# Kernel tuning notes

Measured on AMD Instinct MI355X. Metric: run time of the kernel, lower is better.

## Reference

```python
import jax, jax.numpy as jnp
import numpy as np

N_NODES = 33
EPS = 1e-5


def _tconv(x, w, b):
    # x: (B,T,N,Ci); w: (3,O,Ci,1,ks); b: (3,O). Gated temporal conv: relu(P*sigmoid(Q)+R)
    xt = jnp.transpose(x, (0, 3, 2, 1))  # (B,Ci,N,T)
    def c(i):
        y = jax.lax.conv_general_dilated(xt, w[i], (1, 1), 'VALID',
                                         dimension_numbers=('NCHW', 'OIHW', 'NCHW'))
        return y + b[i][None, :, None, None]
    P, Q, R = c(0), c(1), c(2)
    H = jax.nn.relu(P * jax.nn.sigmoid(Q) + R)
    return jnp.transpose(H, (0, 3, 2, 1))  # (B,T',N,O)


def _cheb(x, edge_index, Wk, bias):
    # ChebConv K=3, sym normalization, lambda_max=2 => L_hat = -D^{-1/2} A D^{-1/2} (diag cancels)
    src, tgt = edge_index[0], edge_index[1]
    w = jnp.ones((src.shape[0],), x.dtype)
    deg = jnp.zeros((N_NODES,), x.dtype).at[src].add(w)
    dinv = jnp.where(deg > 0, deg ** -0.5, 0.0)
    lap_w = -dinv[src] * w * dinv[tgt]

    def prop(z):  # z: (B,T,N,C); sparse matvec over edges, aggregate at target
        zg = z[:, :, src, :] * lap_w[None, None, :, None]
        return jnp.zeros_like(z).at[:, :, tgt, :].add(zg)

    Tx0 = x
    Tx1 = prop(Tx0)
    Tx2 = 2.0 * prop(Tx1) - Tx0
    out = (jnp.einsum('btnc,cd->btnd', Tx0, Wk[0])
           + jnp.einsum('btnc,cd->btnd', Tx1, Wk[1])
           + jnp.einsum('btnc,cd->btnd', Tx2, Wk[2]))
    return out + bias


def _bn(x, g, b):
    # BatchNorm2d(num_nodes): stats per node over (B,T,C); biased variance, train-mode stats
    mean = x.mean(axis=(0, 1, 3), keepdims=True)
    var = x.var(axis=(0, 1, 3), keepdims=True)
    return (x - mean) * jax.lax.rsqrt(var + EPS) * g[None, None, :, None] + b[None, None, :, None]


def _stconv(x, ei, tc1w, tc1b, cw, cb, tc2w, tc2b, bng, bnb):
    t = _tconv(x, tc1w, tc1b)
    t = jax.nn.relu(_cheb(t, ei, cw, cb))
    t = _tconv(t, tc2w, tc2b)
    return _bn(t, bng, bnb)


def setup_inputs() -> dict:
    key = jax.random.key(0)
    ks = jax.random.split(key, 24)
    s = 0.05
    inp = {
        'x': jax.random.normal(ks[0], (32, 512, 33, 3), jnp.float32),
        'edge_index': jax.random.randint(ks[1], (2, 64), 0, 33, jnp.int64) if jax.config.jax_enable_x64 else jax.random.randint(ks[1], (2, 64), 0, 33).astype(jnp.int32),
        # STConv 1 (in=3, hid=out=64)
        's1_tc1_w': jax.random.normal(ks[2], (3, 64, 3, 1, 3), jnp.float32) * s,
        's1_tc1_b': jax.random.normal(ks[3], (3, 64), jnp.float32) * s,
        's1_cheb_w': jax.random.normal(ks[4], (3, 64, 64), jnp.float32) * s,
        's1_cheb_b': jax.random.normal(ks[5], (64,), jnp.float32) * s,
        's1_tc2_w': jax.random.normal(ks[6], (3, 64, 64, 1, 3), jnp.float32) * s,
        's1_tc2_b': jax.random.normal(ks[7], (3, 64), jnp.float32) * s,
        's1_bn_g': jnp.ones((33,), jnp.float32),
        's1_bn_b': jnp.zeros((33,), jnp.float32),
        # STConv 2 (in=64, hid=out=64)
        's2_tc1_w': jax.random.normal(ks[8], (3, 64, 64, 1, 3), jnp.float32) * s,
        's2_tc1_b': jax.random.normal(ks[9], (3, 64), jnp.float32) * s,
        's2_cheb_w': jax.random.normal(ks[10], (3, 64, 64), jnp.float32) * s,
        's2_cheb_b': jax.random.normal(ks[11], (64,), jnp.float32) * s,
        's2_tc2_w': jax.random.normal(ks[12], (3, 64, 64, 1, 3), jnp.float32) * s,
        's2_tc2_b': jax.random.normal(ks[13], (3, 64), jnp.float32) * s,
        's2_bn_g': jnp.ones((33,), jnp.float32),
        's2_bn_b': jnp.zeros((33,), jnp.float32),
        # classifier: Linear(64*33 -> 256), Linear(256 -> 10)
        'fc1_w': jax.random.normal(ks[14], (64 * 33, 256), jnp.float32) * s,
        'fc1_b': jax.random.normal(ks[15], (256,), jnp.float32) * s,
        'fc2_w': jax.random.normal(ks[16], (256, 10), jnp.float32) * s,
        'fc2_b': jax.random.normal(ks[17], (10,), jnp.float32) * s,
    }
    return inp


def reference(x, edge_index,
              s1_tc1_w, s1_tc1_b, s1_cheb_w, s1_cheb_b, s1_tc2_w, s1_tc2_b, s1_bn_g, s1_bn_b,
              s2_tc1_w, s2_tc1_b, s2_cheb_w, s2_cheb_b, s2_tc2_w, s2_tc2_b, s2_bn_g, s2_bn_b,
              fc1_w, fc1_b, fc2_w, fc2_b):
    h = jax.nn.relu(_stconv(x, edge_index, s1_tc1_w, s1_tc1_b, s1_cheb_w, s1_cheb_b,
                            s1_tc2_w, s1_tc2_b, s1_bn_g, s1_bn_b))
    h = jax.nn.relu(_stconv(h, edge_index, s2_tc1_w, s2_tc1_b, s2_cheb_w, s2_cheb_b,
                            s2_tc2_w, s2_tc2_b, s2_bn_g, s2_bn_b))
    h = h.mean(axis=1)                      # (B, N, C) mean over time
    h = h.reshape(h.shape[0], -1)           # (B, N*C)
    h = jax.nn.relu(h @ fc1_w + fc1_b)      # dropout = identity (eval)
    return h @ fc2_w + fc2_b                # (B, num_classes)
```

## Files before the change

kernel.cpp:

```cpp
#include <hip/hip_runtime.h>
#include <math.h>

#define NN 33
#define NC 2112

typedef __attribute__((ext_vector_type(8))) short bfrag;
typedef __attribute__((ext_vector_type(4))) float f32x4;

#define OFF_LT   0
#define OFF_L2T  2244
#define OFF_UP1  4488
#define OFF_UP2  16776
#define OFF_WT0  29064
#define OFF_WT1  65928
#define OFF_WT2  102792
#define OFF_ST1  139656
#define OFF_ST2  139722
#define OFF_HB   139856
#define OFF_MEAN 148048
#define OFF_A    215632
#define A_ELEMS  34332672ull
#define SLAB     1077120ull

__device__ inline unsigned short f2bf(float x) {
  unsigned int u = __float_as_uint(x);
  unsigned int r = (u + 0x7fffu + ((u >> 16) & 1u)) >> 16;
  return (unsigned short)r;
}
__device__ inline float bf2f(unsigned short h) {
  return __uint_as_float(((unsigned int)h) << 16);
}

__global__ __launch_bounds__(256) void k_prep_lap(
    const int* __restrict__ ei, float* __restrict__ ws) {
  __shared__ float Lsm[1089];
  __shared__ float L2sm[1089];
  __shared__ float deg[NN];
  __shared__ float dinv[NN];
  int tid = threadIdx.x;
  for (int i = tid; i < 1089; i += 256) Lsm[i] = 0.f;
  if (tid < NN) deg[tid] = 0.f;
  __syncthreads();
  if (tid < 64) atomicAdd(&deg[ei[tid]], 1.f);
  __syncthreads();
  if (tid < NN) dinv[tid] = deg[tid] > 0.f ? rsqrtf(deg[tid]) : 0.f;
  __syncthreads();
  if (tid < 64) {
    int s = ei[tid], t = ei[64 + tid];
    atomicAdd(&Lsm[t * NN + s], -dinv[s] * dinv[t]);
  }
  __syncthreads();
  for (int i = tid; i < 1089; i += 256) {
    int r = i / NN, c = i % NN;
    float s = 0.f;
    for (int m = 0; m < NN; m++) s += Lsm[r * NN + m] * Lsm[m * NN + c];
    L2sm[i] = 2.f * s;
  }
  __syncthreads();
  for (int i = tid; i < 33 * 66; i += 256) {
    int m = i / 66, nn = i % 66;
    int n33 = nn < 33 ? nn : nn - 33;
    ws[OFF_LT + m * 68 + nn]  = Lsm[n33 * NN + m];
    ws[OFF_L2T + m * 68 + nn] = L2sm[n33 * NN + m];
  }
}

__global__ __launch_bounds__(256) void k_prep_w(
    const float* __restrict__ cw1, const float* __restrict__ cw2,
    const float* __restrict__ tw0, const float* __restrict__ tw1,
    const float* __restrict__ tw2, float* __restrict__ ws) {
  int u = blockIdx.x * 256 + threadIdx.x;
  if (u < 24576) {
    unsigned short* u1 = (unsigned short*)(ws + OFF_UP1);
    unsigned short* u2 = (unsigned short*)(ws + OFF_UP2);
    int j = u & 7;
    int nn = (u >> 3) & 15;
    int q = (u >> 7) & 3;
    int sp = (u >> 9) & 1;
    int blk = u >> 10;
    int nt = blk & 3;
    int ks = blk >> 2;
    int k = ks * 32 + q * 8 + j;
    int d = nt * 16 + nn;
    int s = k >> 6, cc = k & 63;
    float v1 = cw1[(s * 64 + cc) * 64 + d];
    float v2 = cw2[(s * 64 + cc) * 64 + d];
    if (s == 0) { v1 -= cw1[(128 + cc) * 64 + d]; v2 -= cw2[(128 + cc) * 64 + d]; }
    unsigned short h1 = f2bf(v1);
    u1[u] = sp ? f2bf(v1 - bf2f(h1)) : h1;
    unsigned short h2 = f2bf(v2);
    u2[u] = sp ? f2bf(v2 - bf2f(h2)) : h2;
  }
  {
    unsigned short* p0 = (unsigned short*)(ws + OFF_WT0);
    unsigned short* p1 = (unsigned short*)(ws + OFF_WT1);
    unsigned short* p2 = (unsigned short*)(ws + OFF_WT2);
    int j  = u & 7;
    int nn_ = (u >> 3) & 15;
    int q  = (u >> 7) & 3;
    int B  = u >> 9;
    int sp = B & 1;
    int B2 = B >> 1;
    int nt = B2 % 12;
    int dk = B2 / 12;
    int ks = dk & 1;
    int dt = dk >> 1;
    int o  = nt * 16 + nn_;
    int ci = ks * 32 + q * 8 + j;
    int src = (o * 64 + ci) * 3 + dt;
    float w0 = tw0[src], w1 = tw1[src], w2 = tw2[src];
    unsigned short h;
    h = f2bf(w0); p0[u] = sp ? f2bf(w0 - bf2f(h)) : h;
    h = f2bf(w1); p1[u] = sp ? f2bf(w1 - bf2f(h)) : h;
    h = f2bf(w2); p2[u] = sp ? f2bf(w2 - bf2f(h)) : h;
  }
}

__global__ __launch_bounds__(256) void k_tconv0(
    const float* __restrict__ x, const float* __restrict__ w,
    const float* __restrict__ bias, float* __restrict__ out,
    int b0, int total) {
  __shared__ float wsm[1728];
  __shared__ float bsm[192];
  int tid = threadIdx.x;
  for (int i = tid; i < 1728; i += 256) wsm[i] = w[i];
  if (tid < 192) bsm[tid] = bias[tid];
  __syncthreads();
  int idx = blockIdx.x * 256 + tid;
  if (idx >= total) return;
  int ch = idx & 63;
  int r = idx >> 6;
  int n = r % NN; r /= NN;
  int t = r % 510;
  int bc = r / 510;
  int b = b0 + bc;
  float aP = bsm[ch], aQ = bsm[64 + ch], aR = bsm[128 + ch];
  const float* xp = x + ((size_t)(b * 512 + t) * NN + n) * 3;
  #pragma unroll
  for (int dt = 0; dt < 3; dt++) {
    float x0 = xp[dt * 99 + 0], x1 = xp[dt * 99 + 1], x2 = xp[dt * 99 + 2];
    aP += x0 * wsm[(ch * 3 + 0) * 3 + dt] + x1 * wsm[(ch * 3 + 1) * 3 + dt] + x2 * wsm[(ch * 3 + 2) * 3 + dt];
    aQ += x0 * wsm[((64 + ch) * 3 + 0) * 3 + dt] + x1 * wsm[((64 + ch) * 3 + 1) * 3 + dt] + x2 * wsm[((64 + ch) * 3 + 2) * 3 + dt];
    aR += x0 * wsm[((128 + ch) * 3 + 0) * 3 + dt] + x1 * wsm[((128 + ch) * 3 + 1) * 3 + dt] + x2 * wsm[((128 + ch) * 3 + 2) * 3 + dt];
  }
  float sg = 1.f / (1.f + __expf(-aQ));
  out[(size_t)(bc * 510 + t) * NC + n * 64 + ch] = fmaxf(aP * sg + aR, 0.f);
}

__global__ __launch_bounds__(256, 4) void k_chebmm(
    const float* __restrict__ in, const unsigned short* __restrict__ Uf,
    const float* __restrict__ cbias, float* __restrict__ out,
    const float* __restrict__ ws, int totalRows) {
  __shared__ __attribute__((aligned(16))) unsigned short Zh[64 * 136];
  __shared__ __attribute__((aligned(16))) unsigned short Zl[64 * 136];

  int tid = threadIdx.x;
  int R0 = blockIdx.x * 64;
  int c = tid & 63;
  int g = __builtin_amdgcn_readfirstlane(tid >> 6);
  int Rg = R0 + g * 16;
  int btg = Rg / 33;
  int n0 = Rg - btg * 33;
  int wrap = 33 - n0;

  const float* lt  = ws + OFF_LT;
  const float* l2t = ws + OFF_L2T;
  const float* ipA = in + (size_t)btg * NC + c;
  const float* ipB = ipA + NC;
  float z1[16], z2[16];
  #pragma unroll
  for (int rr = 0; rr < 16; rr++) { z1[rr] = 0.f; z2[rr] = 0.f; }
  #pragma unroll 11
  for (int m = 0; m < NN; m++) {
    float hvA = ipA[m * 64];
    float hvB = ipB[m * 64];
    const float* ltm  = lt + m * 68 + n0;
    const float* l2tm = l2t + m * 68 + n0;
    #pragma unroll
    for (int rr = 0; rr < 16; rr++) {
      float hv = (rr < wrap) ? hvA : hvB;
      z1[rr] += ltm[rr] * hv;
      z2[rr] += l2tm[rr] * hv;
    }
  }
  #pragma unroll
  for (int rr = 0; rr < 16; rr++) {
    int r = g * 16 + rr;
    unsigned short zh1 = f2bf(z1[rr]);
    Zh[r * 136 + c] = zh1;
    Zl[r * 136 + c] = f2bf(z1[rr] - bf2f(zh1));
    unsigned short zh2 = f2bf(z2[rr]);
    Zh[r * 136 + 64 + c] = zh2;
    Zl[r * 136 + 64 + c] = f2bf(z2[rr] - bf2f(zh2));
  }

  int lane = tid & 63;
  int m15 = lane & 15, q = lane >> 4;
  f32x4 acc[4];
  #pragma unroll
  for (int nt = 0; nt < 4; nt++) acc[nt] = (f32x4){0.f, 0.f, 0.f, 0.f};

  const float* hrow = in + (size_t)(Rg + m15) * 64 + q * 8;
  float hv0[8], hv1[8];
  *(float4*)&hv0[0] = *(const float4*)(hrow);
  *(float4*)&hv0[4] = *(const float4*)(hrow + 4);
  *(float4*)&hv1[0] = *(const float4*)(hrow + 32);
  *(float4*)&hv1[4] = *(const float4*)(hrow + 36);

  bfrag uh[4], ul[4];
  #pragma unroll
  for (int nt = 0; nt < 4; nt++) {
    const unsigned short* bp = Uf + nt * 1024 + lane * 8;
    uh[nt] = *(const bfrag*)bp;
    ul[nt] = *(const bfrag*)(bp + 512);
  }

  #pragma unroll
  for (int ks = 0; ks < 6; ks++) {
    bfrag nh[4], nl[4];
    if (ks < 5) {
      #pragma unroll
      for (int nt = 0; nt < 4; nt++) {
        const unsigned short* bp = Uf + ((ks + 1) * 4 + nt) * 1024 + lane * 8;
        nh[nt] = *(const bfrag*)bp;
        nl[nt] = *(const bfrag*)(bp + 512);
      }
    }
    bfrag ah, al;
    if (ks < 2) {
      const float* hv = (ks == 0) ? hv0 : hv1;
      union { bfrag v; unsigned short s[8]; } Ahf, Alf;
      #pragma unroll
      for (int j = 0; j < 8; j++) {
        unsigned short hh = f2bf(hv[j]);
        Ahf.s[j] = hh;
        Alf.s[j] = f2bf(hv[j] - bf2f(hh));
      }
      ah = Ahf.v; al = Alf.v;
    } else {
      int aoff = (g * 16 + m15) * 136 + (ks - 2) * 32 + q * 8;
      ah = *(const bfrag*)(Zh + aoff);
      al = *(const bfrag*)(Zl + aoff);
    }
    #pragma unroll
    for (int nt = 0; nt < 4; nt++) {
      acc[nt] = __builtin_amdgcn_mfma_f32_16x16x32_bf16(ah, uh[nt], acc[nt], 0, 0, 0);
      acc[nt] = __builtin_amdgcn_mfma_f32_16x16x32_bf16(ah, ul[nt], acc[nt], 0, 0, 0);
      acc[nt] = __builtin_amdgcn_mfma_f32_16x16x32_bf16(al, uh[nt], acc[nt], 0, 0, 0);
    }
    #pragma unroll
    for (int nt = 0; nt < 4; nt++) { uh[nt] = nh[nt]; ul[nt] = nl[nt]; }
  }
  #pragma unroll
  for (int nt = 0; nt < 4; nt++) {
    int d = nt * 16 + m15;
    float bd = cbias[d];
    #pragma unroll
    for (int rr = 0; rr < 4; rr++) {
      int R = R0 + g * 16 + q * 4 + rr;
      if (R < totalRows)
        out[(size_t)R * 64 + d] = fmaxf(acc[nt][rr] + bd, 0.f);
    }
  }
}

__global__ __launch_bounds__(256, 4) void k_tconv(
    const float* __restrict__ in, int inStride, int Tin,
    const unsigned short* __restrict__ wsp, const float* __restrict__ bias,
    float* __restrict__ out, int outStride, int Tout,
    const float* __restrict__ bnSt, const float* __restrict__ bnG,
    const float* __restrict__ bnB, float bnCnt, float* __restrict__ statsOut) {
  __shared__ __attribute__((aligned(16))) unsigned short Ah[34 * 72];
  __shared__ __attribute__((aligned(16))) unsigned short Al[34 * 72];
  __shared__ float red[8];
  int tid = threadIdx.x;
  int ntt = (Tout + 31) >> 5;
  int tpb = NN * ntt;
  int bc = blockIdx.x / tpb, r = blockIdx.x % tpb;
  int n = r / ntt, tt = r % ntt;
  int t0 = tt << 5;
  const float* ip = in + (size_t)bc * inStride * NC + n * 64;

  float sc = 1.f, sh = 0.f;
  if (bnSt) {
    float mean = bnSt[n] / bnCnt;
    float var = bnSt[33 + n] / bnCnt - mean * mean;
    sc = rsqrtf(var + 1e-5f) * bnG[n];
    sh = bnB[n] - mean * sc;
  }
  for (int i = tid; i < 34 * 16; i += 256) {
    int row = i >> 4, c4 = i & 15;
    float4 v = make_float4(0.f, 0.f, 0.f, 0.f);
    if (t0 + row < Tin) v = *(const float4*)(ip + (size_t)(t0 + row) * NC + c4 * 4);
    if (bnSt) {
      v.x = fmaxf(v.x * sc + sh, 0.f);
      v.y = fmaxf(v.y * sc + sh, 0.f);
      v.z = fmaxf(v.z * sc + sh, 0.f);
      v.w = fmaxf(v.w * sc + sh, 0.f);
    }
    unsigned short h0 = f2bf(v.x), h1 = f2bf(v.y), h2 = f2bf(v.z), h3 = f2bf(v.w);
    unsigned short l0 = f2bf(v.x - bf2f(h0)), l1 = f2bf(v.y - bf2f(h1));
    unsigned short l2 = f2bf(v.z - bf2f(h2)), l3 = f2bf(v.w - bf2f(h3));
    uint2 ph, pl;
    ph.x = (unsigned)h0 | ((unsigned)h1 << 16); ph.y = (unsigned)h2 | ((unsigned)h3 << 16);
    pl.x = (unsigned)l0 | ((unsigned)l1 << 16); pl.y = (unsigned)l2 | ((unsigned)l3 << 16);
    *(uint2*)(Ah + row * 72 + c4 * 4) = ph;
    *(uint2*)(Al + row * 72 + c4 * 4) = pl;
  }
  __syncthreads();

  int lane = tid & 63;
  int wv = tid >> 6;
  int m15 = lane & 15, q = lane >> 4;

  f32x4 acc[2][3];
  #pragma unroll
  for (int mi = 0; mi < 2; mi++)
    #pragma unroll
    for (int j = 0; j < 3; j++) acc[mi][j] = (f32x4){0.f, 0.f, 0.f, 0.f};

  #pragma unroll
  for (int s = 0; s < 6; s++) {
    int dt = s >> 1, ks = s & 1;
    const unsigned short* wdt = wsp + (size_t)dt * 24576;
    bfrag bh[3], bl[3];
    #pragma unroll
    for (int j = 0; j < 3; j++) {
      int nt = wv + 4 * j;
      const unsigned short* bp = wdt + ((ks * 12 + nt) * 2) * 512 + lane * 8;
      bh[j] = *(const bfrag*)bp;
      bl[j] = *(const bfrag*)(bp + 512);
    }
    bfrag ah[2], al[2];
    #pragma unroll
    for (int mi = 0; mi < 2; mi++) {
      int row = mi * 16 + m15 + dt;
      int off = row * 72 + ks * 32 + q * 8;
      ah[mi] = *(const bfrag*)(Ah + off);
      al[mi] = *(const bfrag*)(Al + off);
    }
    #pragma unroll
    for (int j = 0; j < 3; j++)
      #pragma unroll
      for (int mi = 0; mi < 2; mi++) {
        acc[mi][j] = __builtin_amdgcn_mfma_f32_16x16x32_bf16(ah[mi], bh[j], acc[mi][j], 0, 0, 0);
        acc[mi][j] = __builtin_amdgcn_mfma_f32_16x16x32_bf16(ah[mi], bl[j], acc[mi][j], 0, 0, 0);
        acc[mi][j] = __builtin_amdgcn_mfma_f32_16x16x32_bf16(al[mi], bh[j], acc[mi][j], 0, 0, 0);
      }
  }

  float ssum = 0.f, sq = 0.f;
  int ch = wv * 16 + m15;
  float bP = bias[ch], bQ = bias[64 + ch], bR = bias[128 + ch];
  #pragma unroll
  for (int mi = 0; mi < 2; mi++) {
    #pragma unroll
    for (int rr = 0; rr < 4; rr++) {
      int t = t0 + mi * 16 + q * 4 + rr;
      float P = acc[mi][0][rr] + bP;
      float Q = acc[mi][1][rr] + bQ;
      float Rv = acc[mi][2][rr] + bR;
      float sg = 1.f / (1.f + __expf(-Q));
      float h = fmaxf(P * sg + Rv, 0.f);
      if (t < Tout) {
        out[(size_t)(bc * outStride + t) * NC + n * 64 + ch] = h;
        ssum += h; sq += h * h;
      }
    }
  }
  if (statsOut) {
    #pragma unroll
    for (int d = 32; d > 0; d >>= 1) {
      ssum += __shfl_down(ssum, d);
      sq += __shfl_down(sq, d);
    }
    if (lane == 0) { red[wv] = ssum; red[4 + wv] = sq; }
    __syncthreads();
    if (tid == 0) {
      atomicAdd(&statsOut[n], red[0] + red[1] + red[2] + red[3]);
      atomicAdd(&statsOut[33 + n], red[4] + red[5] + red[6] + red[7]);
    }
  }
}

__global__ __launch_bounds__(256) void k_bnmean(
    const float* __restrict__ A, int stride, int Tv,
    const float* __restrict__ st, const float* __restrict__ gg,
    const float* __restrict__ bb, float* __restrict__ mout) {
  int idx = blockIdx.x * 256 + threadIdx.x;
  int p = idx % NC, b = idx / NC;
  int n = p >> 6;
  float cnt = (float)(32 * Tv * 64);
  float mean = st[n] / cnt;
  float var = st[33 + n] / cnt - mean * mean;
  float sc = rsqrtf(var + 1e-5f) * gg[n];
  float sh = bb[n] - mean * sc;
  float acc = 0.f;
  const float* ap = A + (size_t)b * stride * NC + p;
  for (int t = 0; t < Tv; t += 4) {
    acc += fmaxf(ap[(size_t)t * NC] * sc + sh, 0.f)
         + fmaxf(ap[(size_t)(t + 1) * NC] * sc + sh, 0.f)
         + fmaxf(ap[(size_t)(t + 2) * NC] * sc + sh, 0.f)
         + fmaxf(ap[(size_t)(t + 3) * NC] * sc + sh, 0.f);
  }
  mout[idx] = acc / (float)Tv;
}

__global__ __launch_bounds__(256) void k_fc1(
    const float* __restrict__ meanb, const float* __restrict__ w1,
    float* __restrict__ hb) {
  int b = blockIdx.x >> 3, ks = blockIdx.x & 7;
  int d = threadIdx.x;
  const float* mp = meanb + b * NC + ks * 264;
  const float* wp = w1 + (size_t)(ks * 264) * 256 + d;
  float acc = 0.f;
  for (int k = 0; k < 264; k += 8) {
    #pragma unroll
    for (int u = 0; u < 8; u++)
      acc += mp[k + u] * wp[(size_t)(k + u) * 256];
  }
  atomicAdd(&hb[b * 256 + d], acc);
}

__global__ __launch_bounds__(256) void k_fc2(
    const float* __restrict__ hb, const float* __restrict__ b1,
    const float* __restrict__ w2, const float* __restrict__ b2,
    float* __restrict__ out) {
  __shared__ float h[256];
  int tid = threadIdx.x, b = blockIdx.x;
  h[tid] = fmaxf(hb[b * 256 + tid] + b1[tid], 0.f);
  __syncthreads();
  if (tid < 10) {
    float a = b2[tid];
    for (int k = 0; k < 256; k++) a += h[k] * w2[k * 10 + tid];
    out[b * 10 + tid] = a;
  }
}

extern "C" void kernel_launch(void* const* d_in, const int* in_sizes, int n_in,
                              void* d_out, int out_size, void* d_ws, size_t ws_size,
                              hipStream_t stream) {
  const float* x        = (const float*)d_in[0];
  const int*   ei       = (const int*)d_in[1];
  const float* s1_tc1_w = (const float*)d_in[2];
  const float* s1_tc1_b = (const float*)d_in[3];
  const float* s1_cheb_w= (const float*)d_in[4];
  const float* s1_cheb_b= (const float*)d_in[5];
  const float* s1_tc2_w = (const float*)d_in[6];
  const float* s1_tc2_b = (const float*)d_in[7];
  const float* s1_bn_g  = (const float*)d_in[8];
  const float* s1_bn_b  = (const float*)d_in[9];
  const float* s2_tc1_w = (const float*)d_in[10];
  const float* s2_tc1_b = (const float*)d_in[11];
  const float* s2_cheb_w= (const float*)d_in[12];
  const float* s2_cheb_b= (const float*)d_in[13];
  const float* s2_tc2_w = (const float*)d_in[14];
  const float* s2_tc2_b = (const float*)d_in[15];
  const float* s2_bn_g  = (const float*)d_in[16];
  const float* s2_bn_b  = (const float*)d_in[17];
  const float* fc1_w    = (const float*)d_in[18];
  const float* fc1_b    = (const float*)d_in[19];
  const float* fc2_w    = (const float*)d_in[20];
  const float* fc2_b    = (const float*)d_in[21];
  float* ws  = (float*)d_ws;
  float* out = (float*)d_out;

  int chunk = 8;
  while (chunk > 1 &&
         ((size_t)OFF_A + A_ELEMS + (size_t)chunk * SLAB * 2) * 4 > ws_size)
    chunk >>= 1;
  float* A  = ws + OFF_A;
  float* HS = A + A_ELEMS;
  float* CS = HS + (size_t)chunk * SLAB;

  hipMemsetAsync(ws + OFF_ST1, 0, (OFF_HB + 8192 - OFF_ST1) * sizeof(float), stream);
  k_prep_lap<<<1, 256, 0, stream>>>(ei, ws);
  k_prep_w<<<288, 256, 0, stream>>>(s1_cheb_w, s2_cheb_w,
                                    s1_tc2_w, s2_tc1_w, s2_tc2_w, ws);

  const unsigned short* wt0 = (const unsigned short*)(ws + OFF_WT0);
  const unsigned short* wt1 = (const unsigned short*)(ws + OFF_WT1);
  const unsigned short* wt2 = (const unsigned short*)(ws + OFF_WT2);
  const unsigned short* uf1 = (const unsigned short*)(ws + OFF_UP1);
  const unsigned short* uf2 = (const unsigned short*)(ws + OFF_UP2);

  int nchunks = 32 / chunk;
  int rowsC = chunk * 510 * NN;
  int nblkC = (rowsC + 63) / 64;
  float cnt1 = (float)(32 * 508 * 64);
  for (int ci = 0; ci < nchunks; ci++) {
    int b0 = ci * chunk;
    int total0 = chunk * 510 * NC;
    k_tconv0<<<(total0 + 255) / 256, 256, 0, stream>>>(x, s1_tc1_w, s1_tc1_b,
                                                       HS, b0, total0);
    k_chebmm<<<nblkC, 256, 0, stream>>>(HS, uf1, s1_cheb_b, CS, ws, rowsC);
    k_tconv<<<chunk * NN * 16, 256, 0, stream>>>(CS, 510, 510, wt0, s1_tc2_b,
                                                 A + (size_t)b0 * 508 * NC, 508, 508,
                                                 nullptr, nullptr, nullptr, 1.f,
                                                 ws + OFF_ST1);
  }
  for (int ci = 0; ci < nchunks; ci++) {
    int b0 = ci * chunk;
    k_tconv<<<chunk * NN * 16, 256, 0, stream>>>(A + (size_t)b0 * 508 * NC, 508, 508,
                                                 wt1, s2_tc1_b, HS, 510, 506,
                                                 ws + OFF_ST1, s1_bn_g, s1_bn_b, cnt1,
                                                 nullptr);
    k_chebmm<<<nblkC, 256, 0, stream>>>(HS, uf2, s2_cheb_b, CS, ws, rowsC);
    k_tconv<<<chunk * NN * 16, 256, 0, stream>>>(CS, 510, 506, wt2, s2_tc2_b,
                                                 A + (size_t)b0 * 508 * NC, 508, 504,
                                                 nullptr, nullptr, nullptr, 1.f,
                                                 ws + OFF_ST2);
  }
  k_bnmean<<<(32 * NC) / 256, 256, 0, stream>>>(A, 508, 504, ws + OFF_ST2,
                                                s2_bn_g, s2_bn_b, ws + OFF_MEAN);
  k_fc1<<<256, 256, 0, stream>>>(ws + OFF_MEAN, fc1_w, ws + OFF_HB);
  k_fc2<<<32, 256, 0, stream>>>(ws + OFF_HB, fc1_b, fc2_w, fc2_b, out);
}
```

Measured before the change: 1.394 ms.

## Emit Cheb output as node-major bf16 hi/lo split, feed tconv directly from global

The Chebyshev matmul kernel now writes its ReLU output as two bf16 planes (high and residual low) in a node-major [n][b*t][c] layout instead of fp32 rows. A new temporal-conv kernel reads MFMA A fragments straight from global memory in that layout, skipping the LDS staging and the fp32-to-bf16 split. It also covers 64 time steps per block instead of 32. The BN-input temporal conv becomes its own specialised kernel. This cuts conversion work and traffic for the intermediate, at the cost of uncoalesced scattered 2-byte stores in chebmm and overlapping global fragment reads in tconv.

```diff
diff --git a/kernel.cpp b/kernel.cpp
--- a/kernel.cpp
+++ b/kernel.cpp
@@ -149,8 +149,9 @@
 
 __global__ __launch_bounds__(256, 4) void k_chebmm(
     const float* __restrict__ in, const unsigned short* __restrict__ Uf,
-    const float* __restrict__ cbias, float* __restrict__ out,
-    const float* __restrict__ ws, int totalRows) {
+    const float* __restrict__ cbias,
+    unsigned short* __restrict__ csh, unsigned short* __restrict__ csl,
+    int S, const float* __restrict__ ws, int totalRows) {
   __shared__ __attribute__((aligned(16))) unsigned short Zh[64 * 136];
   __shared__ __attribute__((aligned(16))) unsigned short Zl[64 * 136];
 
@@ -251,71 +252,46 @@
     #pragma unroll
     for (int nt = 0; nt < 4; nt++) { uh[nt] = nh[nt]; ul[nt] = nl[nt]; }
   }
-  #pragma unroll
-  for (int nt = 0; nt < 4; nt++) {
-    int d = nt * 16 + m15;
-    float bd = cbias[d];
-    #pragma unroll
-    for (int rr = 0; rr < 4; rr++) {
-      int R = R0 + g * 16 + q * 4 + rr;
-      if (R < totalRows)
-        out[(size_t)R * 64 + d] = fmaxf(acc[nt][rr] + bd, 0.f);
-    }
-  }
-}
-
-__global__ __launch_bounds__(256, 4) void k_tconv(
-    const float* __restrict__ in, int inStride, int Tin,
-    const unsigned short* __restrict__ wsp, const float* __restrict__ bias,
+  float bd[4];
+  #pragma unroll
+  for (int nt = 0; nt < 4; nt++) bd[nt] = cbias[nt * 16 + m15];
+  #pragma unroll
+  for (int rr = 0; rr < 4; rr++) {
+    int R = R0 + g * 16 + q * 4 + rr;
+    if (R < totalRows) {
+      int bt = R / 33, n = R - bt * 33;
+      size_t base = ((size_t)n * S + bt) * 64 + m15;
+      #pragma unroll
+      for (int nt = 0; nt < 4; nt++) {
+        float h = fmaxf(acc[nt][rr] + bd[nt], 0.f);
+        unsigned short hh = f2bf(h);
+        csh[base + nt * 16] = hh;
+        csl[base + nt * 16] = f2bf(h - bf2f(hh));
+      }
+    }
+  }
+}
+
+__global__ __launch_bounds__(256, 4) void k_tconv_d(
+    const unsigned short* __restrict__ csh, const unsigned short* __restrict__ csl,
+    int S, const unsigned short* __restrict__ wsp, const float* __restrict__ bias,
     float* __restrict__ out, int outStride, int Tout,
-    const float* __restrict__ bnSt, const float* __restrict__ bnG,
-    const float* __restrict__ bnB, float bnCnt, float* __restrict__ statsOut) {
-  __shared__ __attribute__((aligned(16))) unsigned short Ah[34 * 72];
-  __shared__ __attribute__((aligned(16))) unsigned short Al[34 * 72];
+    float* __restrict__ statsOut) {
   __shared__ float red[8];
   int tid = threadIdx.x;
-  int ntt = (Tout + 31) >> 5;
+  int ntt = (Tout + 63) >> 6;
   int tpb = NN * ntt;
   int bc = blockIdx.x / tpb, r = blockIdx.x % tpb;
   int n = r / ntt, tt = r % ntt;
-  int t0 = tt << 5;
-  const float* ip = in + (size_t)bc * inStride * NC + n * 64;
-
-  float sc = 1.f, sh = 0.f;
-  if (bnSt) {
-    float mean = bnSt[n] / bnCnt;
-    float var = bnSt[33 + n] / bnCnt - mean * mean;
-    sc = rsqrtf(var + 1e-5f) * bnG[n];
-    sh = bnB[n] - mean * sc;
-  }
-  for (int i = tid; i < 34 * 16; i += 256) {
-    int row = i >> 4, c4 = i & 15;
-    float4 v = make_float4(0.f, 0.f, 0.f, 0.f);
-    if (t0 + row < Tin) v = *(const float4*)(ip + (size_t)(t0 + row) * NC + c4 * 4);
-    if (bnSt) {
-      v.x = fmaxf(v.x * sc + sh, 0.f);
-      v.y = fmaxf(v.y * sc + sh, 0.f);
-      v.z = fmaxf(v.z * sc + sh, 0.f);
-      v.w = fmaxf(v.w * sc + sh, 0.f);
-    }
-    unsigned short h0 = f2bf(v.x), h1 = f2bf(v.y), h2 = f2bf(v.z), h3 = f2bf(v.w);
-    unsigned short l0 = f2bf(v.x - bf2f(h0)), l1 = f2bf(v.y - bf2f(h1));
-    unsigned short l2 = f2bf(v.z - bf2f(h2)), l3 = f2bf(v.w - bf2f(h3));
-    uint2 ph, pl;
-    ph.x = (unsigned)h0 | ((unsigned)h1 << 16); ph.y = (unsigned)h2 | ((unsigned)h3 << 16);
-    pl.x = (unsigned)l0 | ((unsigned)l1 << 16); pl.y = (unsigned)l2 | ((unsigned)l3 << 16);
-    *(uint2*)(Ah + row * 72 + c4 * 4) = ph;
-    *(uint2*)(Al + row * 72 + c4 * 4) = pl;
-  }
-  __syncthreads();
-
+  int t0 = tt << 6;
   int lane = tid & 63;
   int wv = tid >> 6;
   int m15 = lane & 15, q = lane >> 4;
-
-  f32x4 acc[2][3];
-  #pragma unroll
-  for (int mi = 0; mi < 2; mi++)
+  size_t rowbase = ((size_t)n * S + bc * 510 + t0 + m15) * 64 + q * 8;
+
+  f32x4 acc[4][3];
+  #pragma unroll
+  for (int mi = 0; mi < 4; mi++)
     #pragma unroll
     for (int j = 0; j < 3; j++) acc[mi][j] = (f32x4){0.f, 0.f, 0.f, 0.f};
 
@@ -331,18 +307,17 @@
       bh[j] = *(const bfrag*)bp;
       bl[j] = *(const bfrag*)(bp + 512);
     }
-    bfrag ah[2], al[2];
-    #pragma unroll
-    for (int mi = 0; mi < 2; mi++) {
-      int row = mi * 16 + m15 + dt;
-      int off = row * 72 + ks * 32 + q * 8;
-      ah[mi] = *(const bfrag*)(Ah + off);
-      al[mi] = *(const bfrag*)(Al + off);
+    bfrag ah[4], al[4];
+    #pragma unroll
+    for (int mi = 0; mi < 4; mi++) {
+      size_t aoff = rowbase + (size_t)(mi * 16 + dt) * 64 + ks * 32;
+      ah[mi] = *(const bfrag*)(csh + aoff);
+      al[mi] = *(const bfrag*)(csl + aoff);
     }
     #pragma unroll
     for (int j = 0; j < 3; j++)
       #pragma unroll
-      for (int mi = 0; mi < 2; mi++) {
+      for (int mi = 0; mi < 4; mi++) {
         acc[mi][j] = __builtin_amdgcn_mfma_f32_16x16x32_bf16(ah[mi], bh[j], acc[mi][j], 0, 0, 0);
         acc[mi][j] = __builtin_amdgcn_mfma_f32_16x16x32_bf16(ah[mi], bl[j], acc[mi][j], 0, 0, 0);
         acc[mi][j] = __builtin_amdgcn_mfma_f32_16x16x32_bf16(al[mi], bh[j], acc[mi][j], 0, 0, 0);
@@ -353,7 +328,7 @@
   int ch = wv * 16 + m15;
   float bP = bias[ch], bQ = bias[64 + ch], bR = bias[128 + ch];
   #pragma unroll
-  for (int mi = 0; mi < 2; mi++) {
+  for (int mi = 0; mi < 4; mi++) {
     #pragma unroll
     for (int rr = 0; rr < 4; rr++) {
       int t = t0 + mi * 16 + q * 4 + rr;
@@ -368,17 +343,112 @@
       }
     }
   }
-  if (statsOut) {
-    #pragma unroll
-    for (int d = 32; d > 0; d >>= 1) {
-      ssum += __shfl_down(ssum, d);
-      sq += __shfl_down(sq, d);
-    }
-    if (lane == 0) { red[wv] = ssum; red[4 + wv] = sq; }
-    __syncthreads();
-    if (tid == 0) {
-      atomicAdd(&statsOut[n], red[0] + red[1] + red[2] + red[3]);
-      atomicAdd(&statsOut[33 + n], red[4] + red[5] + red[6] + red[7]);
+  #pragma unroll
+  for (int d = 32; d > 0; d >>= 1) {
+    ssum += __shfl_down(ssum, d);
+    sq += __shfl_down(sq, d);
+  }
+  if (lane == 0) { red[wv] = ssum; red[4 + wv] = sq; }
+  __syncthreads();
+  if (tid == 0) {
+    atomicAdd(&statsOut[n], red[0] + red[1] + red[2] + red[3]);
+    atomicAdd(&statsOut[33 + n], red[4] + red[5] + red[6] + red[7]);
+  }
+}
+
+__global__ __launch_bounds__(256, 4) void k_tconv_bn(
+    const float* __restrict__ in, int inStride, int Tin,
+    const unsigned short* __restrict__ wsp, const float* __restrict__ bias,
+    float* __restrict__ out, int outStride, int Tout,
+    const float* __restrict__ bnSt, const float* __restrict__ bnG,
+    const float* __restrict__ bnB, float bnCnt) {
+  __shared__ __attribute__((aligned(16))) unsigned short Ah[34 * 72];
+  __shared__ __attribute__((aligned(16))) unsigned short Al[34 * 72];
+  int tid = threadIdx.x;
+  int ntt = (Tout + 31) >> 5;
+  int tpb = NN * ntt;
+  int bc = blockIdx.x / tpb, r = blockIdx.x % tpb;
+  int n = r / ntt, tt = r % ntt;
+  int t0 = tt << 5;
+  const float* ip = in + (size_t)bc * inStride * NC + n * 64;
+
+  float mean = bnSt[n] / bnCnt;
+  float var = bnSt[33 + n] / bnCnt - mean * mean;
+  float sc = rsqrtf(var + 1e-5f) * bnG[n];
+  float sh = bnB[n] - mean * sc;
+  for (int i = tid; i < 34 * 16; i += 256) {
+    int row = i >> 4, c4 = i & 15;
+    float4 v = make_float4(0.f, 0.f, 0.f, 0.f);
+    if (t0 + row < Tin) v = *(const float4*)(ip + (size_t)(t0 + row) * NC + c4 * 4);
+    v.x = fmaxf(v.x * sc + sh, 0.f);
+    v.y = fmaxf(v.y * sc + sh, 0.f);
+    v.z = fmaxf(v.z * sc + sh, 0.f);
+    v.w = fmaxf(v.w * sc + sh, 0.f);
+    unsigned short h0 = f2bf(v.x), h1 = f2bf(v.y), h2 = f2bf(v.z), h3 = f2bf(v.w);
+    unsigned short l0 = f2bf(v.x - bf2f(h0)), l1 = f2bf(v.y - bf2f(h1));
+    unsigned short l2 = f2bf(v.z - bf2f(h2)), l3 = f2bf(v.w - bf2f(h3));
+    uint2 ph, pl;
+    ph.x = (unsigned)h0 | ((unsigned)h1 << 16); ph.y = (unsigned)h2 | ((unsigned)h3 << 16);
+    pl.x = (unsigned)l0 | ((unsigned)l1 << 16); pl.y = (unsigned)l2 | ((unsigned)l3 << 16);
+    *(uint2*)(Ah + row * 72 + c4 * 4) = ph;
+    *(uint2*)(Al + row * 72 + c4 * 4) = pl;
+  }
+  __syncthreads();
+
+  int lane = tid & 63;
+  int wv = tid >> 6;
+  int m15 = lane & 15, q = lane >> 4;
+
+  f32x4 acc[2][3];
+  #pragma unroll
+  for (int mi = 0; mi < 2; mi++)
+    #pragma unroll
+    for (int j = 0; j < 3; j++) acc[mi][j] = (f32x4){0.f, 0.f, 0.f, 0.f};
+
+  #pragma unroll
+  for (int s = 0; s < 6; s++) {
+    int dt = s >> 1, ks = s & 1;
+    const unsigned short* wdt = wsp + (size_t)dt * 24576;
+    bfrag bh[3], bl[3];
+    #pragma unroll
+    for (int j = 0; j < 3; j++) {
+      int nt = wv + 4 * j;
+      const unsigned short* bp = wdt + ((ks * 12 + nt) * 2) * 512 + lane * 8;
+      bh[j] = *(const bfrag*)bp;
+      bl[j] = *(const bfrag*)(bp + 512);
+    }
+    bfrag ah[2], al[2];
+    #pragma unroll
+    for (int mi = 0; mi < 2; mi++) {
+      int row = mi * 16 + m15 + dt;
+      int off = row * 72 + ks * 32 + q * 8;
+      ah[mi] = *(const bfrag*)(Ah + off);
+      al[mi] = *(const bfrag*)(Al + off);
+    }
+    #pragma unroll
+    for (int j = 0; j < 3; j++)
+      #pragma unroll
+      for (int mi = 0; mi < 2; mi++) {
+        acc[mi][j] = __builtin_amdgcn_mfma_f32_16x16x32_bf16(ah[mi], bh[j], acc[mi][j], 0, 0, 0);
+        acc[mi][j] = __builtin_amdgcn_mfma_f32_16x16x32_bf16(ah[mi], bl[j], acc[mi][j], 0, 0, 0);
+        acc[mi][j] = __builtin_amdgcn_mfma_f32_16x16x32_bf16(al[mi], bh[j], acc[mi][j], 0, 0, 0);
+      }
+  }
+
+  int ch = wv * 16 + m15;
+  float bP = bias[ch], bQ = bias[64 + ch], bR = bias[128 + ch];
+  #pragma unroll
+  for (int mi = 0; mi < 2; mi++) {
+    #pragma unroll
+    for (int rr = 0; rr < 4; rr++) {
+      int t = t0 + mi * 16 + q * 4 + rr;
+      float P = acc[mi][0][rr] + bP;
+      float Q = acc[mi][1][rr] + bQ;
+      float Rv = acc[mi][2][rr] + bR;
+      float sg = 1.f / (1.f + __expf(-Q));
+      float h = fmaxf(P * sg + Rv, 0.f);
+      if (t < Tout)
+        out[(size_t)(bc * outStride + t) * NC + n * 64 + ch] = h;
     }
   }
 }
@@ -467,11 +537,14 @@
 
   int chunk = 8;
   while (chunk > 1 &&
-         ((size_t)OFF_A + A_ELEMS + (size_t)chunk * SLAB * 2) * 4 > ws_size)
+         ((size_t)OFF_A + A_ELEMS + (size_t)chunk * SLAB * 2 + 1024) * 4 > ws_size)
     chunk >>= 1;
   float* A  = ws + OFF_A;
   float* HS = A + A_ELEMS;
   float* CS = HS + (size_t)chunk * SLAB;
+  int S = chunk * 510;
+  unsigned short* CSh = (unsigned short*)CS;
+  unsigned short* CSl = CSh + (size_t)chunk * SLAB;
 
   hipMemsetAsync(ws + OFF_ST1, 0, (OFF_HB + 8192 - OFF_ST1) * sizeof(float), stream);
   k_prep_lap<<<1, 256, 0, stream>>>(ei, ws);
@@ -493,23 +566,20 @@
     int total0 = chunk * 510 * NC;
     k_tconv0<<<(total0 + 255) / 256, 256, 0, stream>>>(x, s1_tc1_w, s1_tc1_b,
                                                        HS, b0, total0);
-    k_chebmm<<<nblkC, 256, 0, stream>>>(HS, uf1, s1_cheb_b, CS, ws, rowsC);
-    k_tconv<<<chunk * NN * 16, 256, 0, stream>>>(CS, 510, 510, wt0, s1_tc2_b,
-                                                 A + (size_t)b0 * 508 * NC, 508, 508,
-                                                 nullptr, nullptr, nullptr, 1.f,
-                                                 ws + OFF_ST1);
+    k_chebmm<<<nblkC, 256, 0, stream>>>(HS, uf1, s1_cheb_b, CSh, CSl, S, ws, rowsC);
+    k_tconv_d<<<chunk * NN * 8, 256, 0, stream>>>(CSh, CSl, S, wt0, s1_tc2_b,
+                                                  A + (size_t)b0 * 508 * NC, 508, 508,
+                                                  ws + OFF_ST1);
   }
   for (int ci = 0; ci < nchunks; ci++) {
     int b0 = ci * chunk;
-    k_tconv<<<chunk * NN * 16, 256, 0, stream>>>(A + (size_t)b0 * 508 * NC, 508, 508,
-                                                 wt1, s2_tc1_b, HS, 510, 506,
-                                                 ws + OFF_ST1, s1_bn_g, s1_bn_b, cnt1,
-                                                 nullptr);
-    k_chebmm<<<nblkC, 256, 0, stream>>>(HS, uf2, s2_cheb_b, CS, ws, rowsC);
-    k_tconv<<<chunk * NN * 16, 256, 0, stream>>>(CS, 510, 506, wt2, s2_tc2_b,
-                                                 A + (size_t)b0 * 508 * NC, 508, 504,
-                                                 nullptr, nullptr, nullptr, 1.f,
-                                                 ws + OFF_ST2);
+    k_tconv_bn<<<chunk * NN * 16, 256, 0, stream>>>(A + (size_t)b0 * 508 * NC, 508, 508,
+                                                    wt1, s2_tc1_b, HS, 510, 506,
+                                                    ws + OFF_ST1, s1_bn_g, s1_bn_b, cnt1);
+    k_chebmm<<<nblkC, 256, 0, stream>>>(HS, uf2, s2_cheb_b, CSh, CSl, S, ws, rowsC);
+    k_tconv_d<<<chunk * NN * 8, 256, 0, stream>>>(CSh, CSl, S, wt2, s2_tc2_b,
+                                                  A + (size_t)b0 * 508 * NC, 508, 504,
+                                                  ws + OFF_ST2);
   }
   k_bnmean<<<(32 * NC) / 256, 256, 0, stream>>>(A, 508, 504, ws + OFF_ST2,
                                                 s2_bn_g, s2_bn_b, ws + OFF_MEAN);
```

After: 1.601 ms. 1.15x slower.
